# Kernel tuning notes

Measured on AMD Instinct MI355X. Metric: run time of the kernel, lower is better.

## Reference

```python
import jax, jax.numpy as jnp
import numpy as np

NUM_HEADS = 16
HEAD_DIM = 64
HIDDEN = NUM_HEADS * HEAD_DIM


def _rope_tables(seq_len, dim, dtype):
    # inv_freq: [dim/2]; emb = cat(freqs, freqs): [S, dim]
    inv_freq = 1.0 / (10000.0 ** (jnp.arange(0, dim, 2, dtype=jnp.float32) / dim))
    t = jnp.arange(seq_len, dtype=jnp.float32)
    freqs = jnp.einsum('i,j->ij', t, inv_freq)
    emb = jnp.concatenate([freqs, freqs], axis=-1)
    return jnp.cos(emb).astype(dtype), jnp.sin(emb).astype(dtype)  # [S, dim] each


def _rotate_half(x):
    x1, x2 = jnp.split(x, 2, axis=-1)
    return jnp.concatenate([-x2, x1], axis=-1)


def setup_inputs() -> dict:
    key = jax.random.key(0)
    k1, k2, k3, k4 = jax.random.split(key, 4)
    B, S = 2, 2048
    hidden_states = jax.random.normal(k1, (B, S, HIDDEN), dtype=jnp.float32)
    scale = 0.02
    Wq = jax.random.normal(k2, (HIDDEN, HIDDEN), dtype=jnp.float32) * scale
    Wk = jax.random.normal(k3, (HIDDEN, HIDDEN), dtype=jnp.float32) * scale
    Wv = jax.random.normal(k4, (HIDDEN, HIDDEN), dtype=jnp.float32) * scale
    return {"hidden_states": hidden_states, "Wq": Wq, "Wk": Wk, "Wv": Wv}


def reference(hidden_states, Wq, Wk, Wv):
    B, S, H = hidden_states.shape
    # nn.Linear: x @ W.T ; reshape to [B, heads, S, head_dim]
    def split_heads(x):
        return x.reshape(B, S, NUM_HEADS, HEAD_DIM).transpose(0, 2, 1, 3)
    q = split_heads(hidden_states @ Wq.T)
    k = split_heads(hidden_states @ Wk.T)
    v = split_heads(hidden_states @ Wv.T)
    # inline RoPE over full head_dim
    cos, sin = _rope_tables(S, HEAD_DIM, q.dtype)  # [S, head_dim]
    cos = cos[None, None]  # [1,1,S,head_dim]
    sin = sin[None, None]
    q = q * cos + _rotate_half(q) * sin
    k = k * cos + _rotate_half(k) * sin
    # manual softmax attention
    scores = jnp.einsum('bhqd,bhkd->bhqk', q, k) / (HEAD_DIM ** 0.5)
    probs = jax.nn.softmax(scores, axis=-1)
    ctx = jnp.einsum('bhqk,bhkd->bhqd', probs, v)
    ctx = ctx.transpose(0, 2, 1, 3).reshape(B, S, H)
    return ctx
```

## Files before the change

### kernel.cpp

```cpp
#include <hip/hip_runtime.h>
#include <math.h>

#define NHEADS 16
#define HDIM   64
#define HID    1024
#define BATCH  2
#define SEQ    2048
#define NX (BATCH*SEQ*HID)
#define NW (HID*HID)

typedef unsigned short u16;
typedef __attribute__((ext_vector_type(8))) short  bf16x8;
typedef __attribute__((ext_vector_type(8))) unsigned short u16x8;
typedef __attribute__((ext_vector_type(4))) float  f32x4;


__device__ __forceinline__ void split8(const float* xf, bf16x8& hi, bf16x8& lo) {
    unsigned* hp = (unsigned*)&hi;
    unsigned* lp = (unsigned*)&lo;
#pragma unroll
    for (int j = 0; j < 4; j++) {
        const float p0 = xf[2 * j], p1 = xf[2 * j + 1];
        const unsigned u0 = __float_as_uint(p0);
        const unsigned u1 = __float_as_uint(p1);
        hp[j] = __builtin_amdgcn_perm(u1, u0, 0x07060302u);
        const float l0 = p0 - __uint_as_float(u0 & 0xFFFF0000u);
        const float l1 = p1 - __uint_as_float(u1 & 0xFFFF0000u);
        lp[j] = __builtin_amdgcn_perm(__float_as_uint(l1), __float_as_uint(l0), 0x07060302u);
    }
}
__device__ __forceinline__ void split1(float v, u16& h, u16& l) {
    unsigned u = __float_as_uint(v);
    h = (u16)(u >> 16);
    l = (u16)(__float_as_uint(v - __uint_as_float(u & 0xFFFF0000u)) >> 16);
}

__global__ void rope_tables_kernel(float* __restrict__ ct, float* __restrict__ st) {
    int idx = blockIdx.x * 256 + threadIdx.x;
    if (idx >= SEQ * HDIM) return;
    int s  = idx >> 6;
    int dh = idx & 63;
    int i  = dh & 31;
    float inv = exp2f(-(float)i * (13.28771237954945f / 32.0f));
    float fr  = (float)s * inv;
    ct[idx] = cosf(fr);
    st[idx] = sinf(fr);
}

__global__ void split_kernel(const float* __restrict__ X,
                             const float* __restrict__ W0,
                             const float* __restrict__ W1,
                             const float* __restrict__ W2,
                             u16* __restrict__ Xhi, u16* __restrict__ Xlo,
                             u16* __restrict__ Whi, u16* __restrict__ Wlo)
{
    long idx = ((long)blockIdx.x * 256 + threadIdx.x) * 4;
    if (idx >= (long)NX + 3L * NW) return;
    const float* src; u16* dh; u16* dl; long off;
    if (idx < NX) { src = X; dh = Xhi; dl = Xlo; off = idx; }
    else {
        long rr = idx - NX;
        int wi = (int)(rr >> 20);
        off = rr & (NW - 1);
        src = (wi == 0) ? W0 : ((wi == 1) ? W1 : W2);
        dh = Whi + (size_t)wi * NW;
        dl = Wlo + (size_t)wi * NW;
    }
    const int r = (int)(off >> 10);
    const int k = (int)(off & 1023);
    const size_t fo = ((size_t)(r >> 4) * 32 + (k >> 5)) * 512
                    + (size_t)((k >> 3) & 3) * 128 + (size_t)(r & 15) * 8 + (k & 7);
    float4 v = *(const float4*)(src + off);
    const float* vf = (const float*)&v;
    ushort4 h4, l4;
    u16* hp = (u16*)&h4; u16* lp = (u16*)&l4;
#pragma unroll
    for (int e = 0; e < 4; e++) split1(vf[e], hp[e], lp[e]);
    *(ushort4*)(dh + fo) = h4;
    *(ushort4*)(dl + fo) = l4;
}

__global__ __launch_bounds__(256, 2) void qkv_mfma_kernel(
    const u16* __restrict__ Xhi, const u16* __restrict__ Xlo,
    const u16* __restrict__ Whi, const u16* __restrict__ Wlo,
    const float* __restrict__ ct, const float* __restrict__ st,
    u16* __restrict__ Qhi, u16* __restrict__ Qlo,
    u16* __restrict__ Khi, u16* __restrict__ Klo,
    u16* __restrict__ Vhi, u16* __restrict__ Vlo)
{
    __shared__ unsigned vtr[64][129];

    const int t    = threadIdx.x;
    const int lane = t & 63;
    const int w    = t >> 6;
    const int lx   = lane & 15;
    const int quad = lane >> 4;

    const int lid  = blockIdx.x;
    const int xcd  = lid & 7;
    const int i_   = lid >> 3;
    const int proj = i_ % 3;
    const int mb   = i_ / 3;
    const int nb   = xcd;
    const int n0   = nb * 128;
    const int m0   = mb * 128;

    const u16* __restrict__ Wph = Whi + (size_t)proj * NW;
    const u16* __restrict__ Wpl = Wlo + (size_t)proj * NW;

    const int am = (w & 1) * 64;
    const int bn = (w >> 1) * 64;
    const int lp = quad * 128 + lx * 8;

    const u16 *pAh[4], *pAl[4], *pBh[4], *pBl[4];
#pragma unroll
    for (int i = 0; i < 4; i++) {
        const size_t o = ((size_t)(((m0 + am) >> 4) + i) * 32) * 512 + lp;
        pAh[i] = Xhi + o; pAl[i] = Xlo + o;
    }
#pragma unroll
    for (int j = 0; j < 4; j++) {
        const size_t o = ((size_t)(((n0 + bn) >> 4) + j) * 32) * 512 + lp;
        pBh[j] = Wph + o; pBl[j] = Wpl + o;
    }

    f32x4 acc[4][4];
#pragma unroll
    for (int i = 0; i < 4; i++)
#pragma unroll
        for (int j = 0; j < 4; j++) acc[i][j] = (f32x4){0.f, 0.f, 0.f, 0.f};

    bf16x8 cah[4], cal[4], cbh[4], cbl[4];
    bf16x8 nah[4], nal[4], nbh[4], nbl[4];
#pragma unroll
    for (int i = 0; i < 4; i++) { cah[i] = *(const bf16x8*)(pAh[i]); cal[i] = *(const bf16x8*)(pAl[i]); }
#pragma unroll
    for (int j = 0; j < 4; j++) { cbh[j] = *(const bf16x8*)(pBh[j]); cbl[j] = *(const bf16x8*)(pBl[j]); }

#pragma unroll 1
    for (int kt = 0; kt < HID; kt += 64) {
        const int ko1 = ((kt + 32) >> 5) * 512;
        const int ko2 = (kt + 64 < HID) ? ((kt + 64) >> 5) * 512 : 0;

#pragma unroll
        for (int i = 0; i < 4; i++) { nah[i] = *(const bf16x8*)(pAh[i] + ko1); nal[i] = *(const bf16x8*)(pAl[i] + ko1); }
#pragma unroll
        for (int j = 0; j < 4; j++) { nbh[j] = *(const bf16x8*)(pBh[j] + ko1); nbl[j] = *(const bf16x8*)(pBl[j] + ko1); }

        __builtin_amdgcn_s_setprio(1);
#pragma unroll
        for (int j = 0; j < 4; j++)
#pragma unroll
            for (int i = 0; i < 4; i++) {
                acc[i][j] = __builtin_amdgcn_mfma_f32_16x16x32_bf16(cah[i], cbh[j], acc[i][j], 0, 0, 0);
                acc[i][j] = __builtin_amdgcn_mfma_f32_16x16x32_bf16(cal[i], cbh[j], acc[i][j], 0, 0, 0);
                acc[i][j] = __builtin_amdgcn_mfma_f32_16x16x32_bf16(cah[i], cbl[j], acc[i][j], 0, 0, 0);
            }
        __builtin_amdgcn_s_setprio(0);

#pragma unroll
        for (int i = 0; i < 4; i++) { cah[i] = *(const bf16x8*)(pAh[i] + ko2); cal[i] = *(const bf16x8*)(pAl[i] + ko2); }
#pragma unroll
        for (int j = 0; j < 4; j++) { cbh[j] = *(const bf16x8*)(pBh[j] + ko2); cbl[j] = *(const bf16x8*)(pBl[j] + ko2); }

        __builtin_amdgcn_s_setprio(1);
#pragma unroll
        for (int j = 0; j < 4; j++)
#pragma unroll
            for (int i = 0; i < 4; i++) {
                acc[i][j] = __builtin_amdgcn_mfma_f32_16x16x32_bf16(nah[i], nbh[j], acc[i][j], 0, 0, 0);
                acc[i][j] = __builtin_amdgcn_mfma_f32_16x16x32_bf16(nal[i], nbh[j], acc[i][j], 0, 0, 0);
                acc[i][j] = __builtin_amdgcn_mfma_f32_16x16x32_bf16(nah[i], nbl[j], acc[i][j], 0, 0, 0);
            }
        __builtin_amdgcn_s_setprio(0);
    }

    const int b      = m0 >> 11;
    const int head   = (n0 >> 6) + (w >> 1);
    const int m_base = m0 + am;

    if (proj < 2) {
#pragma unroll
        for (int i = 0; i < 4; i++) {
#pragma unroll
            for (int r = 0; r < 4; r++) {
                const int s = (m_base + i * 16 + quad * 4 + r) & 2047;
                const float* ctr = ct + s * HDIM;
                const float* str = st + s * HDIM;
                float nv[4];
#pragma unroll
                for (int j = 0; j < 4; j++) {
                    const int dh = j * 16 + lx;
                    const float c  = ctr[dh];
                    const float sn = str[dh];
                    const float x  = acc[i][j][r];
                    const float p  = acc[i][j ^ 2][r];
                    nv[j] = (j < 2) ? (x * c - p * sn) : (x * c + p * sn);
                }
#pragma unroll
                for (int j = 0; j < 4; j++) acc[i][j][r] = nv[j];
            }
        }
        u16* dh_ = (proj == 0) ? Qhi : Khi;
        u16* dl_ = (proj == 0) ? Qlo : Klo;
        const float qscale = (proj == 0) ? 0.18033688011112042f : 1.0f;
        const size_t obase = (size_t)(b * NHEADS + head) * SEQ * HDIM;
#pragma unroll
        for (int i = 0; i < 4; i++)
#pragma unroll
            for (int r = 0; r < 4; r++) {
                const int s   = (m_base + i * 16 + quad * 4 + r) & 2047;
                const int rb  = s >> 4;
                const int lxq = s & 15;
#pragma unroll
                for (int j = 0; j < 4; j++) {
                    const size_t fo = obase + ((size_t)rb * 2 + (j >> 1)) * 512
                                    + (size_t)((j & 1) * 2 + (lx >> 3)) * 128
                                    + (size_t)lxq * 8 + (lx & 7);
                    u16 hh, ll;
                    split1(acc[i][j][r] * qscale, hh, ll);
                    dh_[fo] = hh;
                    dl_[fo] = ll;
                }
            }
    } else {
#pragma unroll 1
        for (int pass = 0; pass < 2; pass++) {
            __syncthreads();
            if ((w & 1) == pass) {
#pragma unroll
                for (int i = 0; i < 4; i++)
#pragma unroll
                    for (int j = 0; j < 4; j++)
#pragma unroll
                        for (int r = 0; r < 4; r++) {
                            const int ml = i * 16 + quad * 4 + r;
                            const int nl = bn + j * 16 + lx;
                            const float v = acc[i][j][r];
                            unsigned u  = __float_as_uint(v);
                            unsigned hi = u & 0xFFFF0000u;
                            unsigned lo = __float_as_uint(v - __uint_as_float(hi)) >> 16;
                            vtr[ml][nl] = hi | lo;
                        }
            }
            __syncthreads();
            {
                const int d      = t >> 1;
                const int sh     = (t & 1) * 32;
                const int headv  = (n0 >> 6) + (d >> 6);
                const int dd     = d & 63;
                const size_t vbase = (size_t)(b * NHEADS + headv) * SEQ * HDIM;
                const int s0base = (m0 & 2047) + pass * 64 + sh;
#pragma unroll
                for (int k = 0; k < 4; k++) {
                    const int s0 = s0base + k * 8;
                    u16x8 hv, lv;
#pragma unroll
                    for (int e = 0; e < 8; e++) {
                        unsigned u = vtr[sh + k * 8 + e][d];
                        hv[e] = (u16)(u >> 16);
                        lv[e] = (u16)(u & 0xFFFFu);
                    }
                    const size_t fo = vbase + ((size_t)(dd >> 4) * 64 + (s0 >> 5)) * 512
                                    + (size_t)((s0 >> 3) & 3) * 128 + (size_t)(dd & 15) * 8;
                    *(u16x8*)(Vhi + fo) = hv;
                    *(u16x8*)(Vlo + fo) = lv;
                }
            }
        }
    }
}

__global__ __launch_bounds__(256, 2) void attn_kernel(
    const u16* __restrict__ Qhi, const u16* __restrict__ Qlo,
    const u16* __restrict__ Khi, const u16* __restrict__ Klo,
    const u16* __restrict__ Vhi, const u16* __restrict__ Vlo,
    float* __restrict__ OUT)
{
    __shared__ float PS[4][32][68];

    const int t    = threadIdx.x;
    const int lane = t & 63;
    const int w    = t >> 6;
    const int lx   = lane & 15;
    const int quad = lane >> 4;

    const int q0 = blockIdx.x * 128;
    const int h  = blockIdx.y;
    const int b  = blockIdx.z;
    const size_t base = (size_t)(b * NHEADS + h) * SEQ * HDIM;
    const int lp = quad * 128 + lx * 8;

    bf16x8 qh[2][2], ql[2][2];
#pragma unroll
    for (int a = 0; a < 2; a++)
#pragma unroll
        for (int ks = 0; ks < 2; ks++) {
            const size_t fo = base + ((size_t)((q0 >> 4) + w * 2 + a) * 2 + ks) * 512 + lp;
            qh[a][ks] = *(const bf16x8*)(Qhi + fo);
            ql[a][ks] = *(const bf16x8*)(Qlo + fo);
        }

    f32x4 O[2][4];
    float l_part[2][4];
#pragma unroll
    for (int a = 0; a < 2; a++) {
#pragma unroll
        for (int dt = 0; dt < 4; dt++) O[a][dt] = (f32x4){0.f,0.f,0.f,0.f};
#pragma unroll
        for (int r = 0; r < 4; r++) l_part[a][r] = 0.f;
    }

    bf16x8 kAh[2][4], kAl[2][4], kBh[2][4], kBl[2][4];
#pragma unroll
    for (int c = 0; c < 4; c++)
#pragma unroll
        for (int ks = 0; ks < 2; ks++) {
            const size_t fo = base + ((size_t)c * 2 + ks) * 512 + lp;
            kAh[ks][c] = *(const bf16x8*)(Khi + fo);
            kAl[ks][c] = *(const bf16x8*)(Klo + fo);
        }

    auto tile_body = [&](bf16x8 (&ckh)[2][4], bf16x8 (&ckl)[2][4],
                         bf16x8 (&nkh)[2][4], bf16x8 (&nkl)[2][4],
                         int kt, int ktn) {
        bf16x8 vh[2][4], vl[2][4];
#pragma unroll
        for (int dt = 0; dt < 4; dt++)
#pragma unroll
            for (int ks2 = 0; ks2 < 2; ks2++) {
                const size_t fo = base + ((size_t)dt * 64 + (kt >> 5) + ks2) * 512 + lp;
                vh[ks2][dt] = *(const bf16x8*)(Vhi + fo);
                vl[ks2][dt] = *(const bf16x8*)(Vlo + fo);
            }

#pragma unroll
        for (int a = 0; a < 2; a++) {
#pragma unroll
            for (int c = 0; c < 4; c++) {
                f32x4 acc = (f32x4){0.f,0.f,0.f,0.f};
                __builtin_amdgcn_s_setprio(1);
#pragma unroll
                for (int ks = 0; ks < 2; ks++) {
                    acc = __builtin_amdgcn_mfma_f32_16x16x32_bf16(qh[a][ks], ckh[ks][c], acc, 0, 0, 0);
                    acc = __builtin_amdgcn_mfma_f32_16x16x32_bf16(ql[a][ks], ckh[ks][c], acc, 0, 0, 0);
                    acc = __builtin_amdgcn_mfma_f32_16x16x32_bf16(qh[a][ks], ckl[ks][c], acc, 0, 0, 0);
                }
                __builtin_amdgcn_s_setprio(0);
#pragma unroll
                for (int r = 0; r < 4; r++) {
                    float p = exp2f(acc[r]);
                    l_part[a][r] += p;
                    PS[w][a * 16 + quad * 4 + r][c * 16 + lx] = p;
                }
            }
        }

#pragma unroll
        for (int c = 0; c < 4; c++)
#pragma unroll
            for (int ks = 0; ks < 2; ks++) {
                const size_t fo = base + ((size_t)((ktn >> 4) + c) * 2 + ks) * 512 + lp;
                nkh[ks][c] = *(const bf16x8*)(Khi + fo);
                nkl[ks][c] = *(const bf16x8*)(Klo + fo);
            }

#pragma unroll
        for (int a = 0; a < 2; a++) {
#pragma unroll
            for (int ks2 = 0; ks2 < 2; ks2++) {
                const float* ps = &PS[w][a * 16 + lx][ks2 * 32 + quad * 8];
                float pf[8];
                *(float4*)&pf[0] = *(const float4*)ps;
                *(float4*)&pf[4] = *(const float4*)(ps + 4);
                bf16x8 phi, plo;
                split8(pf, phi, plo);
                __builtin_amdgcn_s_setprio(1);
#pragma unroll
                for (int dt = 0; dt < 4; dt++) {
                    O[a][dt] = __builtin_amdgcn_mfma_f32_16x16x32_bf16(phi, vh[ks2][dt], O[a][dt], 0, 0, 0);
                    O[a][dt] = __builtin_amdgcn_mfma_f32_16x16x32_bf16(plo, vh[ks2][dt], O[a][dt], 0, 0, 0);
                    O[a][dt] = __builtin_amdgcn_mfma_f32_16x16x32_bf16(phi, vl[ks2][dt], O[a][dt], 0, 0, 0);
                }
                __builtin_amdgcn_s_setprio(0);
            }
        }
    };

#pragma unroll 1
    for (int kt = 0; kt < SEQ; kt += 128) {
        tile_body(kAh, kAl, kBh, kBl, kt,       kt + 64);
        tile_body(kBh, kBl, kAh, kAl, kt + 64, (kt + 128) & (SEQ - 1));
    }

    float linv[2][4];
#pragma unroll
    for (int a = 0; a < 2; a++)
#pragma unroll
        for (int r = 0; r < 4; r++) {
            float l = l_part[a][r];
            l += __shfl_xor(l, 1);
            l += __shfl_xor(l, 2);
            l += __shfl_xor(l, 4);
            l += __shfl_xor(l, 8);
            linv[a][r] = 1.f / l;
        }

    float* Po = &PS[0][0][0];
    __syncthreads();
#pragma unroll
    for (int a = 0; a < 2; a++)
#pragma unroll
        for (int dt = 0; dt < 4; dt++)
#pragma unroll
            for (int r = 0; r < 4; r++)
                Po[(size_t)(w * 32 + a * 16 + quad * 4 + r) * 68 + dt * 16 + lx] =
                    O[a][dt][r] * linv[a][r];
    __syncthreads();
    {
        const int q    = t >> 1;
        const int half = t & 1;
        const float* prow = Po + (size_t)q * 68 + half * 32;
        float* dst = OUT + ((size_t)(b * SEQ + q0 + q)) * HID + h * HDIM + half * 32;
#pragma unroll
        for (int e = 0; e < 8; e++)
            ((float4*)dst)[e] = ((const float4*)prow)[e];
    }
}

extern "C" void kernel_launch(void* const* d_in, const int* in_sizes, int n_in,
                              void* d_out, int out_size, void* d_ws, size_t ws_size,
                              hipStream_t stream)
{
    const float* X  = (const float*)d_in[0];
    const float* Wq = (const float*)d_in[1];
    const float* Wk = (const float*)d_in[2];
    const float* Wv = (const float*)d_in[3];
    float* out = (float*)d_out;

    const size_t qkv_elems = (size_t)BATCH * NHEADS * SEQ * HDIM;
    char* wsb = (char*)d_ws;
    float* ct  = (float*)wsb;
    float* st  = ct + (size_t)SEQ * HDIM;
    u16* Xhi = (u16*)(st + (size_t)SEQ * HDIM);
    u16* Xlo = Xhi + (size_t)NX;
    u16* Whi = Xlo + (size_t)NX;
    u16* Wlo = Whi + 3 * (size_t)NW;
    u16* Qhi = Wlo + 3 * (size_t)NW;
    u16* Qlo = Qhi + qkv_elems;
    u16* Khi = Qlo + qkv_elems;
    u16* Klo = Khi + qkv_elems;
    u16* Vhi = Klo + qkv_elems;
    u16* Vlo = Vhi + qkv_elems;

    rope_tables_kernel<<<(SEQ * HDIM + 255) / 256, 256, 0, stream>>>(ct, st);

    const long tot = (long)NX + 3L * NW;
    split_kernel<<<(int)((tot / 4 + 255) / 256), 256, 0, stream>>>(
        X, Wq, Wk, Wv, Xhi, Xlo, Whi, Wlo);

    qkv_mfma_kernel<<<dim3(3 * (HID / 128) * ((BATCH * SEQ) / 128)), 256, 0, stream>>>(
        Xhi, Xlo, Whi, Wlo, ct, st, Qhi, Qlo, Khi, Klo, Vhi, Vlo);

    attn_kernel<<<dim3(SEQ / 128, NHEADS, BATCH), 256, 0, stream>>>(
        Qhi, Qlo, Khi, Klo, Vhi, Vlo, out);
}
```

Before: 304.0 us.

## Stage K and V-hi tiles through shared memory and vectorize split kernel writes

In the attention kernel, the K hi/lo and V-hi tiles are now loaded cooperatively once per block into LDS and shared by all four waves. Before, each wave loaded them from global memory into registers, so the same tile was fetched four times per block. A register prefetch of the next tile overlaps with compute, but this adds two __syncthreads per 64-key step. V-lo is still read directly from global. The split kernel is also restructured so each thread handles 8 contiguous elements and writes whole 16-byte fragments in the swizzled layout, replacing scattered 8-byte writes.

```diff
diff --git a/kernel.cpp b/kernel.cpp
--- a/kernel.cpp
+++ b/kernel.cpp
@@ -47,37 +47,41 @@
     st[idx] = sinf(fr);
 }
 
-__global__ void split_kernel(const float* __restrict__ X,
-                             const float* __restrict__ W0,
-                             const float* __restrict__ W1,
-                             const float* __restrict__ W2,
-                             u16* __restrict__ Xhi, u16* __restrict__ Xlo,
-                             u16* __restrict__ Whi, u16* __restrict__ Wlo)
+__global__ __launch_bounds__(256) void split_kernel(
+    const float* __restrict__ X,
+    const float* __restrict__ W0,
+    const float* __restrict__ W1,
+    const float* __restrict__ W2,
+    u16* __restrict__ Xhi, u16* __restrict__ Xlo,
+    u16* __restrict__ Whi, u16* __restrict__ Wlo)
 {
-    long idx = ((long)blockIdx.x * 256 + threadIdx.x) * 4;
-    if (idx >= (long)NX + 3L * NW) return;
-    const float* src; u16* dh; u16* dl; long off;
-    if (idx < NX) { src = X; dh = Xhi; dl = Xlo; off = idx; }
+    const int s = blockIdx.x * 4 + (threadIdx.x >> 6);
+    const int l = threadIdx.x & 63;
+    const int r = l & 15, q = l >> 4;
+    const float* src; u16* dh; u16* dl; int so;
+    if (s < 8192) { src = X; dh = Xhi; dl = Xlo; so = s; }
     else {
-        long rr = idx - NX;
-        int wi = (int)(rr >> 20);
-        off = rr & (NW - 1);
+        const int wi = (s - 8192) >> 11;
+        so = (s - 8192) & 2047;
         src = (wi == 0) ? W0 : ((wi == 1) ? W1 : W2);
         dh = Whi + (size_t)wi * NW;
         dl = Wlo + (size_t)wi * NW;
     }
-    const int r = (int)(off >> 10);
-    const int k = (int)(off & 1023);
-    const size_t fo = ((size_t)(r >> 4) * 32 + (k >> 5)) * 512
-                    + (size_t)((k >> 3) & 3) * 128 + (size_t)(r & 15) * 8 + (k & 7);
-    float4 v = *(const float4*)(src + off);
-    const float* vf = (const float*)&v;
-    ushort4 h4, l4;
-    u16* hp = (u16*)&h4; u16* lp = (u16*)&l4;
-#pragma unroll
-    for (int e = 0; e < 4; e++) split1(vf[e], hp[e], lp[e]);
-    *(ushort4*)(dh + fo) = h4;
-    *(ushort4*)(dl + fo) = l4;
+    const int R0 = (so >> 5) << 4, K0 = (so & 31) << 5;
+    const float* sp = src + (size_t)(R0 + r) * 1024 + K0 + q * 8;
+    float v[8];
+    *(float4*)&v[0] = *(const float4*)sp;
+    *(float4*)&v[4] = *(const float4*)(sp + 4);
+    u16x8 h8, l8;
+#pragma unroll
+    for (int e = 0; e < 8; e++) {
+        u16 hh, ll;
+        split1(v[e], hh, ll);
+        h8[e] = hh; l8[e] = ll;
+    }
+    const size_t off = (size_t)so * 512 + l * 8;
+    *(u16x8*)(dh + off) = h8;
+    *(u16x8*)(dl + off) = l8;
 }
 
 __global__ __launch_bounds__(256, 2) void qkv_mfma_kernel(
@@ -277,6 +281,7 @@
     const u16* __restrict__ Vhi, const u16* __restrict__ Vlo,
     float* __restrict__ OUT)
 {
+    __shared__ __align__(16) u16 KVs[3][4096];
     __shared__ float PS[4][32][68];
 
     const int t    = threadIdx.x;
@@ -311,27 +316,50 @@
         for (int r = 0; r < 4; r++) l_part[a][r] = 0.f;
     }
 
-    bf16x8 kAh[2][4], kAl[2][4], kBh[2][4], kBl[2][4];
-#pragma unroll
-    for (int c = 0; c < 4; c++)
-#pragma unroll
-        for (int ks = 0; ks < 2; ks++) {
-            const size_t fo = base + ((size_t)c * 2 + ks) * 512 + lp;
-            kAh[ks][c] = *(const bf16x8*)(Khi + fo);
-            kAl[ks][c] = *(const bf16x8*)(Klo + fo);
-        }
-
-    auto tile_body = [&](bf16x8 (&ckh)[2][4], bf16x8 (&ckl)[2][4],
-                         bf16x8 (&nkh)[2][4], bf16x8 (&nkl)[2][4],
-                         int kt, int ktn) {
-        bf16x8 vh[2][4], vl[2][4];
+    u16x8 sreg[6];
+    auto stage_load = [&](int kt) {
+#pragma unroll
+        for (int i = 0; i < 6; i++) {
+            const int o = (((i & 1) << 8) + t) * 8;
+            const u16* g;
+            if (i < 2)      g = Khi + base + (size_t)(kt >> 4) * 1024 + o;
+            else if (i < 4) g = Klo + base + (size_t)(kt >> 4) * 1024 + o;
+            else {
+                const int dt = o >> 10, rem = o & 1023;
+                g = Vhi + base + ((size_t)dt * 64 + (kt >> 5)) * 512 + rem;
+            }
+            sreg[i] = *(const u16x8*)g;
+        }
+    };
+
+    stage_load(0);
+
+#pragma unroll 1
+    for (int kt = 0; kt < SEQ; kt += 64) {
+        __syncthreads();
+#pragma unroll
+        for (int i = 0; i < 6; i++) {
+            const int o = (((i & 1) << 8) + t) * 8;
+            *(u16x8*)&KVs[i >> 1][o] = sreg[i];
+        }
+        __syncthreads();
+
+        stage_load((kt + 64) & (SEQ - 1));
+
+        bf16x8 vl[2][4];
 #pragma unroll
         for (int dt = 0; dt < 4; dt++)
 #pragma unroll
-            for (int ks2 = 0; ks2 < 2; ks2++) {
-                const size_t fo = base + ((size_t)dt * 64 + (kt >> 5) + ks2) * 512 + lp;
-                vh[ks2][dt] = *(const bf16x8*)(Vhi + fo);
-                vl[ks2][dt] = *(const bf16x8*)(Vlo + fo);
+            for (int ks2 = 0; ks2 < 2; ks2++)
+                vl[ks2][dt] = *(const bf16x8*)(Vlo + base + ((size_t)dt * 64 + (kt >> 5) + ks2) * 512 + lp);
+
+        bf16x8 kh[2][4], kl[2][4];
+#pragma unroll
+        for (int c = 0; c < 4; c++)
+#pragma unroll
+            for (int ks = 0; ks < 2; ks++) {
+                kh[ks][c] = *(const bf16x8*)&KVs[0][(c * 2 + ks) * 512 + lp];
+                kl[ks][c] = *(const bf16x8*)&KVs[1][(c * 2 + ks) * 512 + lp];
             }
 
 #pragma unroll
@@ -342,9 +370,9 @@
                 __builtin_amdgcn_s_setprio(1);
 #pragma unroll
                 for (int ks = 0; ks < 2; ks++) {
-                    acc = __builtin_amdgcn_mfma_f32_16x16x32_bf16(qh[a][ks], ckh[ks][c], acc, 0, 0, 0);
-                    acc = __builtin_amdgcn_mfma_f32_16x16x32_bf16(ql[a][ks], ckh[ks][c], acc, 0, 0, 0);
-                    acc = __builtin_amdgcn_mfma_f32_16x16x32_bf16(qh[a][ks], ckl[ks][c], acc, 0, 0, 0);
+                    acc = __builtin_amdgcn_mfma_f32_16x16x32_bf16(qh[a][ks], kh[ks][c], acc, 0, 0, 0);
+                    acc = __builtin_amdgcn_mfma_f32_16x16x32_bf16(ql[a][ks], kh[ks][c], acc, 0, 0, 0);
+                    acc = __builtin_amdgcn_mfma_f32_16x16x32_bf16(qh[a][ks], kl[ks][c], acc, 0, 0, 0);
                 }
                 __builtin_amdgcn_s_setprio(0);
 #pragma unroll
@@ -356,14 +384,12 @@
             }
         }
 
-#pragma unroll
-        for (int c = 0; c < 4; c++)
-#pragma unroll
-            for (int ks = 0; ks < 2; ks++) {
-                const size_t fo = base + ((size_t)((ktn >> 4) + c) * 2 + ks) * 512 + lp;
-                nkh[ks][c] = *(const bf16x8*)(Khi + fo);
-                nkl[ks][c] = *(const bf16x8*)(Klo + fo);
-            }
+        bf16x8 vh[2][4];
+#pragma unroll
+        for (int dt = 0; dt < 4; dt++)
+#pragma unroll
+            for (int ks2 = 0; ks2 < 2; ks2++)
+                vh[ks2][dt] = *(const bf16x8*)&KVs[2][dt * 1024 + ks2 * 512 + lp];
 
 #pragma unroll
         for (int a = 0; a < 2; a++) {
@@ -385,12 +411,6 @@
                 __builtin_amdgcn_s_setprio(0);
             }
         }
-    };
-
-#pragma unroll 1
-    for (int kt = 0; kt < SEQ; kt += 128) {
-        tile_body(kAh, kAl, kBh, kBl, kt,       kt + 64);
-        tile_body(kBh, kBl, kAh, kAl, kt + 64, (kt + 128) & (SEQ - 1));
     }
 
     float linv[2][4];
@@ -455,8 +475,7 @@
 
     rope_tables_kernel<<<(SEQ * HDIM + 255) / 256, 256, 0, stream>>>(ct, st);
 
-    const long tot = (long)NX + 3L * NW;
-    split_kernel<<<(int)((tot / 4 + 255) / 256), 256, 0, stream>>>(
+    split_kernel<<<3584, 256, 0, stream>>>(
         X, Wq, Wk, Wv, Xhi, Xlo, Whi, Wlo);
 
     qkv_mfma_kernel<<<dim3(3 * (HID / 128) * ((BATCH * SEQ) / 128)), 256, 0, stream>>>(
```

Result: faster. 268.2 us (-11.8%).
